# Optimization experiments

Hardware: AMD Instinct MI355X
Metric: run time of the kernel (lower is better)

## Reference

```python
import jax, jax.numpy as jnp
import numpy as np

DIM = 64
HEADS = 4
WIN = 4


def setup_inputs() -> dict:
    key = jax.random.key(0)
    ks = jax.random.split(key, 9)
    B, C, D, H, W = 2, DIM, 64, 64, 64
    x = jax.random.normal(ks[0], (B, C, D, H, W), dtype=jnp.float32)
    # 1x1x1 Conv3d == pointwise linear: weight [C_out, C_in], bias [C_out]
    def mk(kw, kb):
        return (jax.random.normal(kw, (C, C), dtype=jnp.float32) * 0.05,
                jax.random.normal(kb, (C,), dtype=jnp.float32) * 0.05)
    Wq, bq = mk(ks[1], ks[2])
    Wk, bk = mk(ks[3], ks[4])
    Wv, bv = mk(ks[5], ks[6])
    Wp, bp = mk(ks[7], ks[8])
    return {"x": x, "Wq": Wq, "bq": bq, "Wk": Wk, "bk": bk,
            "Wv": Wv, "bv": bv, "Wp": Wp, "bp": bp}


def reference(x, Wq, bq, Wk, bk, Wv, bv, Wp, bp):
    B, C, D, H, W = x.shape
    w = WIN
    heads = HEADS
    hd = C // heads
    L = w * w * w  # tokens per window (64)
    nd, nh, nw = D // w, H // w, W // w  # spatial dims are multiples of w -> no padding branch
    scale = hd ** -0.5

    # window partition: [B,C,D,H,W] -> [B*nd*nh*nw, C, L]
    xw = (x.reshape(B, C, nd, w, nh, w, nw, w)
            .transpose(0, 2, 4, 6, 1, 3, 5, 7)
            .reshape(B * nd * nh * nw, C, L))

    def pointwise(t, Wm, bm):  # 1x1x1 conv on flattened windows
        return jnp.einsum('ncl,oc->nol', t, Wm) + bm[None, :, None]

    q = pointwise(xw, Wq, bq).reshape(-1, heads, hd, L)
    k = pointwise(xw, Wk, bk).reshape(-1, heads, hd, L)
    v = pointwise(xw, Wv, bv).reshape(-1, heads, hd, L)

    # attn[n,h,i,j] = <q[:, :, :, i], k[:, :, :, j]> * scale ; softmax over j
    attn = jax.nn.softmax(jnp.einsum('nhdi,nhdj->nhij', q, k) * scale, axis=-1)
    # out = v @ attn^T  (dropout is identity in eval)
    out = jnp.einsum('nhdj,nhij->nhdi', v, attn)

    out = out.reshape(-1, C, L)
    out = pointwise(out, Wp, bp)

    # reverse window partition: [B*nd*nh*nw, C, L] -> [B,C,D,H,W]
    out = (out.reshape(B, nd, nh, nw, C, w, w, w)
              .transpose(0, 4, 1, 5, 2, 6, 3, 7)
              .reshape(B, C, D, H, W))
    return out
```

## Files before the change

kernel.cpp:

```cpp
#include <hip/hip_runtime.h>

typedef _Float16 f16;
typedef __attribute__((ext_vector_type(4))) _Float16 f16x4;
typedef __attribute__((ext_vector_type(8))) _Float16 f16x8;
typedef __attribute__((ext_vector_type(4))) float f32x4;

#define MFMA32(a,b,c) __builtin_amdgcn_mfma_f32_16x16x32_f16((a),(b),(c),0,0,0)
#define MFMA16(a,b,c) __builtin_amdgcn_mfma_f32_16x16x16f16((a),(b),(c),0,0,0)

__global__ void wprep(const float* __restrict__ Wq, const float* __restrict__ Wk,
                      const float* __restrict__ Wv, const float* __restrict__ Wp,
                      f16* __restrict__ ws)
{
    const int t = threadIdx.x;
    const int lane = t & 63;
    const float* Wm[4] = {Wq, Wk, Wv, Wp};
    #pragma unroll
    for (int j = 0; j < 8; ++j) {
        const int c = (t >> 6) * 8 + j;
        const int m = c >> 3, ob = (c >> 1) & 3, s = c & 1;
        const float* src = Wm[m] + (ob * 16 + (lane & 15)) * 64 + 8 * (lane >> 4) + 32 * s;
        f32x4 a4 = *(const f32x4*)src;
        f32x4 b4 = *(const f32x4*)(src + 4);
        f16x8 h;
        #pragma unroll
        for (int ii = 0; ii < 8; ++ii) h[ii] = (f16)(ii < 4 ? a4[ii] : b4[ii - 4]);
        *(f16x8*)(ws + c * 512 + lane * 8) = h;
    }
    #pragma unroll
    for (int j = 0; j < 4; ++j) {
        const int f = (t >> 6) * 4 + j;
        const int oc = f >> 2, hh = f & 3;
        f32x4 wv = *(const f32x4*)(Wp + (oc * 16 + (lane & 15)) * 64 + 16 * hh + 4 * (lane >> 4));
        f16x4 h4;
        #pragma unroll
        for (int r = 0; r < 4; ++r) h4[r] = (f16)wv[r];
        *(f16x4*)(ws + 16384 + f * 256 + lane * 4) = h4;
    }
}

__global__ __launch_bounds__(256, 3)
void wsa3d(const float* __restrict__ x, const f16* __restrict__ wsf,
           const float* __restrict__ bq, const float* __restrict__ bk,
           const float* __restrict__ bv, const float* __restrict__ bp,
           float* __restrict__ out)
{
    __shared__ __align__(16) f16 XW[16384];
    float* const SG = (float*)XW;

    const int tid  = threadIdx.x;
    const int lane = tid & 63;
    const int w    = tid >> 6;
    const int g    = lane >> 4;
    const int ln16 = lane & 15;
    const int key  = ln16 & 7;

    const int bid = blockIdx.x;
    const int Q   = ((bid & 7) << 8) | (bid >> 3);
    const int qx = Q & 3, ih = (Q >> 2) & 15, idz = (Q >> 6) & 15, b = Q >> 10;

    const float c_sc = 0.25f * 1.44269504088896340736f;
    const f32x4 z4 = {0.f, 0.f, 0.f, 0.f};
    const f16x4 ones = {(f16)1.f, (f16)1.f, (f16)1.f, (f16)1.f};

    const int gz = (lane >> 4) & 3, gy = (lane >> 2) & 3, gq = lane & 3;

    f16x4 valh[16];
    #pragma unroll
    for (int i = 0; i < 16; ++i) {
        const int c = w * 16 + i;
        f32x4 v4 = *(const f32x4*)(x + ((((b*64 + c)*64 + idz*4 + gz)*64) + ih*4 + gy)*64 + qx*16 + gq*4);
        #pragma unroll
        for (int r = 0; r < 4; ++r) valh[i][r] = (f16)v4[r];
    }

    #pragma unroll
    for (int lx = 0; lx < 4; ++lx) {
        const int t = gz * 16 + gy * 4 + lx;
        #pragma unroll
        for (int h2 = 0; h2 < 2; ++h2) {
            f16x8 pk;
            #pragma unroll
            for (int ii = 0; ii < 8; ++ii) pk[ii] = valh[h2 * 8 + ii][lx];
            *(f16x8*)(XW + gq*4096 + t*64 + (((w*2 + h2) ^ (t & 7) ^ gq) << 3)) = pk;
        }
    }
    __syncthreads();

    f16x8 xf[4][2];
    #pragma unroll
    for (int lb = 0; lb < 4; ++lb)
        #pragma unroll
        for (int s = 0; s < 2; ++s)
            xf[lb][s] = *(const f16x8*)(XW + w*4096 + (lb*16 + ln16)*64 + (((g + 4*s) ^ key ^ w) << 3));

    #pragma unroll
    for (int ob = 0; ob < 4; ++ob) {
        f16x8 VF[2];
        #pragma unroll
        for (int s = 0; s < 2; ++s) VF[s] = *(const f16x8*)(wsf + (16 + ob*2 + s)*512 + lane*8);
        const float bvo = bv[ob * 16 + ln16];
        #pragma unroll
        for (int tb = 0; tb < 4; ++tb) {
            f32x4 a = z4;
            #pragma unroll
            for (int s = 0; s < 2; ++s) a = MFMA32(xf[tb][s], VF[s], a);
            f16x4 h4;
            #pragma unroll
            for (int r = 0; r < 4; ++r) h4[r] = (f16)(a[r] + bvo);
            *(f16x4*)(XW + w*4096 + (ob*16 + ln16)*64 + (((2*tb + (g >> 1)) ^ key ^ w) << 3) + 4*(g & 1)) = h4;
        }
    }

    f16x4 ot[4][4];
    #pragma unroll
    for (int h = 0; h < 4; ++h) {
        f16x8 QF[2], KF[2];
        #pragma unroll
        for (int s = 0; s < 2; ++s) {
            QF[s] = *(const f16x8*)(wsf + (h*2 + s)*512 + lane*8);
            KF[s] = *(const f16x8*)(wsf + (8 + h*2 + s)*512 + lane*8);
        }
        const f32x4 bqv = *(const f32x4*)(bq + h*16 + g*4);
        const f32x4 bkv = *(const f32x4*)(bk + h*16 + g*4);
        f16x4 qf[4], kf[4];
        #pragma unroll
        for (int lb = 0; lb < 4; ++lb) {
            f32x4 aq = z4, ak = z4;
            #pragma unroll
            for (int s = 0; s < 2; ++s) {
                aq = MFMA32(QF[s], xf[lb][s], aq);
                ak = MFMA32(KF[s], xf[lb][s], ak);
            }
            #pragma unroll
            for (int r = 0; r < 4; ++r) {
                qf[lb][r] = (f16)((aq[r] + bqv[r]) * c_sc);
                kf[lb][r] = (f16)(ak[r] + bkv[r]);
            }
        }
        f16x4 va[4];
        #pragma unroll
        for (int jb = 0; jb < 4; ++jb)
            va[jb] = *(const f16x4*)(XW + w*4096 + (16*h + ln16)*64 + (((2*jb + (g >> 1)) ^ key ^ w) << 3) + 4*(g & 1));
        #pragma unroll
        for (int ib = 0; ib < 4; ++ib) {
            f16x4 pf[4];
            #pragma unroll
            for (int jb = 0; jb < 4; ++jb) {
                f32x4 S = MFMA16(kf[jb], qf[ib], z4);
                #pragma unroll
                for (int r = 0; r < 4; ++r) pf[jb][r] = (f16)__builtin_amdgcn_exp2f(S[r]);
            }
            f32x4 sm = z4;
            #pragma unroll
            for (int jb = 0; jb < 4; ++jb) sm = MFMA16(ones, pf[jb], sm);
            f32x4 O = z4;
            #pragma unroll
            for (int jb = 0; jb < 4; ++jb) O = MFMA16(va[jb], pf[jb], O);
            const float inv = __builtin_amdgcn_rcpf(sm[0]);
            #pragma unroll
            for (int r = 0; r < 4; ++r) ot[h][ib][r] = (f16)(O[r] * inv);
        }
    }
    __syncthreads();

    const f16* ws2 = wsf + 16384;
    #pragma unroll
    for (int half = 0; half < 2; ++half) {
        #pragma unroll
        for (int pp = 0; pp < 2; ++pp) {
            const int oc = half * 2 + pp;
            const float bpo = bp[oc * 16 + ln16];
            f16x4 wb[4];
            #pragma unroll
            for (int h = 0; h < 4; ++h)
                wb[h] = *(const f16x4*)(ws2 + (oc * 4 + h) * 256 + lane * 4);
            #pragma unroll
            for (int ib = 0; ib < 4; ++ib) {
                f32x4 a = z4;
                #pragma unroll
                for (int h = 0; h < 4; ++h) a = MFMA16(ot[h][ib], wb[h], a);
                #pragma unroll
                for (int r = 0; r < 4; ++r) a[r] += bpo;
                *(f32x4*)(SG + ((pp*4 + w)*16 + ln16)*64 + (((4*ib + g) ^ ln16 ^ w) << 2)) = a;
            }
        }
        __syncthreads();
        #pragma unroll
        for (int pp = 0; pp < 2; ++pp) {
            const int oc = half * 2 + pp;
            #pragma unroll
            for (int si = 0; si < 4; ++si) {
                const int o2 = w * 4 + si;
                f32x4 v4 = *(const f32x4*)(SG + ((pp*4 + gq)*16 + o2)*64 + (((gz*4 + gy) ^ o2 ^ gq) << 2));
                *(f32x4*)(out + ((((b*64 + oc*16 + o2)*64 + idz*4 + gz)*64) + ih*4 + gy)*64 + qx*16 + gq*4) = v4;
            }
        }
        if (half == 0) __syncthreads();
    }
}

extern "C" void kernel_launch(void* const* d_in, const int* in_sizes, int n_in,
                              void* d_out, int out_size, void* d_ws, size_t ws_size,
                              hipStream_t stream) {
    (void)in_sizes; (void)n_in; (void)out_size; (void)ws_size;
    const float* x  = (const float*)d_in[0];
    const float* Wq = (const float*)d_in[1];
    const float* bq = (const float*)d_in[2];
    const float* Wk = (const float*)d_in[3];
    const float* bk = (const float*)d_in[4];
    const float* Wv = (const float*)d_in[5];
    const float* bv = (const float*)d_in[6];
    const float* Wp = (const float*)d_in[7];
    const float* bp = (const float*)d_in[8];
    f16* wsf = (f16*)d_ws;
    wprep<<<1, 256, 0, stream>>>(Wq, Wk, Wv, Wp, wsf);
    wsa3d<<<2048, 256, 0, stream>>>(x, wsf, bq, bk, bv, bp, (float*)d_out);
}
```

Before: 72.86 us.

## Process two window groups per block and prefetch the second input during compute

Each block now handles two adjacent groups of windows (qx0 and qx1), halving the grid. The global loads for the second group are issued into registers while the first group's attention and projection are still running. The aim is to hide global load latency behind compute. In exchange, register pressure rises (32 extra f32x4 values live), which could lower occupancy or cause spills, and there are fewer blocks per GPU to hide latency.

```diff
diff --git a/kernel.cpp b/kernel.cpp
--- a/kernel.cpp
+++ b/kernel.cpp
@@ -38,6 +38,14 @@
         *(f16x4*)(ws + 16384 + f * 256 + lane * 4) = h4;
     }
 }
+
+#define GATHER16(RAW, B_, IDZ_, IH_, QX_)                                                     \
+    _Pragma("unroll")                                                                         \
+    for (int i = 0; i < 16; ++i) {                                                            \
+        const int c = w * 16 + i;                                                             \
+        RAW[i] = *(const f32x4*)(x + ((((B_*64 + c)*64 + IDZ_*4 + gz)*64) + IH_*4 + gy)*64    \
+                                   + QX_*16 + gq*4);                                          \
+    }
 
 __global__ __launch_bounds__(256, 3)
 void wsa3d(const float* __restrict__ x, const f16* __restrict__ wsf,
@@ -56,23 +64,23 @@
     const int key  = ln16 & 7;
 
     const int bid = blockIdx.x;
-    const int Q   = ((bid & 7) << 8) | (bid >> 3);
-    const int qx = Q & 3, ih = (Q >> 2) & 15, idz = (Q >> 6) & 15, b = Q >> 10;
+    const int Bp  = ((bid & 7) << 7) | (bid >> 3);
+    const int Q0  = Bp * 2;
+    const int qx0 = Q0 & 3, ih = (Q0 >> 2) & 15, idz = (Q0 >> 6) & 15, b = Q0 >> 10;
+    const int qx1 = qx0 | 1;
 
     const float c_sc = 0.25f * 1.44269504088896340736f;
     const f32x4 z4 = {0.f, 0.f, 0.f, 0.f};
     const f16x4 ones = {(f16)1.f, (f16)1.f, (f16)1.f, (f16)1.f};
+    const f16* ws2 = wsf + 16384;
 
     const int gz = (lane >> 4) & 3, gy = (lane >> 2) & 3, gq = lane & 3;
 
-    f16x4 valh[16];
-    #pragma unroll
-    for (int i = 0; i < 16; ++i) {
-        const int c = w * 16 + i;
-        f32x4 v4 = *(const f32x4*)(x + ((((b*64 + c)*64 + idz*4 + gz)*64) + ih*4 + gy)*64 + qx*16 + gq*4);
-        #pragma unroll
-        for (int r = 0; r < 4; ++r) valh[i][r] = (f16)v4[r];
-    }
+    f16x8 xf[4][2];
+    f16x4 ot[4][4];
+    f32x4 raw0[16], raw1[16];
+
+    GATHER16(raw0, b, idz, ih, qx0)
 
     #pragma unroll
     for (int lx = 0; lx < 4; ++lx) {
@@ -81,13 +89,12 @@
         for (int h2 = 0; h2 < 2; ++h2) {
             f16x8 pk;
             #pragma unroll
-            for (int ii = 0; ii < 8; ++ii) pk[ii] = valh[h2 * 8 + ii][lx];
+            for (int ii = 0; ii < 8; ++ii) pk[ii] = (f16)raw0[h2 * 8 + ii][lx];
             *(f16x8*)(XW + gq*4096 + t*64 + (((w*2 + h2) ^ (t & 7) ^ gq) << 3)) = pk;
         }
     }
     __syncthreads();
 
-    f16x8 xf[4][2];
     #pragma unroll
     for (int lb = 0; lb < 4; ++lb)
         #pragma unroll
@@ -112,7 +119,6 @@
         }
     }
 
-    f16x4 ot[4][4];
     #pragma unroll
     for (int h = 0; h < 4; ++h) {
         f16x8 QF[2], KF[2];
@@ -162,9 +168,11 @@
             for (int r = 0; r < 4; ++r) ot[h][ib][r] = (f16)(O[r] * inv);
         }
     }
+
+    GATHER16(raw1, b, idz, ih, qx1)
+
     __syncthreads();
 
-    const f16* ws2 = wsf + 16384;
     #pragma unroll
     for (int half = 0; half < 2; ++half) {
         #pragma unroll
@@ -193,7 +201,129 @@
             for (int si = 0; si < 4; ++si) {
                 const int o2 = w * 4 + si;
                 f32x4 v4 = *(const f32x4*)(SG + ((pp*4 + gq)*16 + o2)*64 + (((gz*4 + gy) ^ o2 ^ gq) << 2));
-                *(f32x4*)(out + ((((b*64 + oc*16 + o2)*64 + idz*4 + gz)*64) + ih*4 + gy)*64 + qx*16 + gq*4) = v4;
+                *(f32x4*)(out + ((((b*64 + oc*16 + o2)*64 + idz*4 + gz)*64) + ih*4 + gy)*64 + qx0*16 + gq*4) = v4;
+            }
+        }
+        __syncthreads();
+    }
+
+    #pragma unroll
+    for (int lx = 0; lx < 4; ++lx) {
+        const int t = gz * 16 + gy * 4 + lx;
+        #pragma unroll
+        for (int h2 = 0; h2 < 2; ++h2) {
+            f16x8 pk;
+            #pragma unroll
+            for (int ii = 0; ii < 8; ++ii) pk[ii] = (f16)raw1[h2 * 8 + ii][lx];
+            *(f16x8*)(XW + gq*4096 + t*64 + (((w*2 + h2) ^ (t & 7) ^ gq) << 3)) = pk;
+        }
+    }
+    __syncthreads();
+
+    #pragma unroll
+    for (int lb = 0; lb < 4; ++lb)
+        #pragma unroll
+        for (int s = 0; s < 2; ++s)
+            xf[lb][s] = *(const f16x8*)(XW + w*4096 + (lb*16 + ln16)*64 + (((g + 4*s) ^ key ^ w) << 3));
+
+    #pragma unroll
+    for (int ob = 0; ob < 4; ++ob) {
+        f16x8 VF[2];
+        #pragma unroll
+        for (int s = 0; s < 2; ++s) VF[s] = *(const f16x8*)(wsf + (16 + ob*2 + s)*512 + lane*8);
+        const float bvo = bv[ob * 16 + ln16];
+        #pragma unroll
+        for (int tb = 0; tb < 4; ++tb) {
+            f32x4 a = z4;
+            #pragma unroll
+            for (int s = 0; s < 2; ++s) a = MFMA32(xf[tb][s], VF[s], a);
+            f16x4 h4;
+            #pragma unroll
+            for (int r = 0; r < 4; ++r) h4[r] = (f16)(a[r] + bvo);
+            *(f16x4*)(XW + w*4096 + (ob*16 + ln16)*64 + (((2*tb + (g >> 1)) ^ key ^ w) << 3) + 4*(g & 1)) = h4;
+        }
+    }
+
+    #pragma unroll
+    for (int h = 0; h < 4; ++h) {
+        f16x8 QF[2], KF[2];
+        #pragma unroll
+        for (int s = 0; s < 2; ++s) {
+            QF[s] = *(const f16x8*)(wsf + (h*2 + s)*512 + lane*8);
+            KF[s] = *(const f16x8*)(wsf + (8 + h*2 + s)*512 + lane*8);
+        }
+        const f32x4 bqv = *(const f32x4*)(bq + h*16 + g*4);
+        const f32x4 bkv = *(const f32x4*)(bk + h*16 + g*4);
+        f16x4 qf[4], kf[4];
+        #pragma unroll
+        for (int lb = 0; lb < 4; ++lb) {
+            f32x4 aq = z4, ak = z4;
+            #pragma unroll
+            for (int s = 0; s < 2; ++s) {
+                aq = MFMA32(QF[s], xf[lb][s], aq);
+                ak = MFMA32(KF[s], xf[lb][s], ak);
+            }
+            #pragma unroll
+            for (int r = 0; r < 4; ++r) {
+                qf[lb][r] = (f16)((aq[r] + bqv[r]) * c_sc);
+                kf[lb][r] = (f16)(ak[r] + bkv[r]);
+            }
+        }
+        f16x4 va[4];
+        #pragma unroll
+        for (int jb = 0; jb < 4; ++jb)
+            va[jb] = *(const f16x4*)(XW + w*4096 + (16*h + ln16)*64 + (((2*jb + (g >> 1)) ^ key ^ w) << 3) + 4*(g & 1));
+        #pragma unroll
+        for (int ib = 0; ib < 4; ++ib) {
+            f16x4 pf[4];
+            #pragma unroll
+            for (int jb = 0; jb < 4; ++jb) {
+                f32x4 S = MFMA16(kf[jb], qf[ib], z4);
+                #pragma unroll
+                for (int r = 0; r < 4; ++r) pf[jb][r] = (f16)__builtin_amdgcn_exp2f(S[r]);
+            }
+            f32x4 sm = z4;
+            #pragma unroll
+            for (int jb = 0; jb < 4; ++jb) sm = MFMA16(ones, pf[jb], sm);
+            f32x4 O = z4;
+            #pragma unroll
+            for (int jb = 0; jb < 4; ++jb) O = MFMA16(va[jb], pf[jb], O);
+            const float inv = __builtin_amdgcn_rcpf(sm[0]);
+            #pragma unroll
+            for (int r = 0; r < 4; ++r) ot[h][ib][r] = (f16)(O[r] * inv);
+        }
+    }
+    __syncthreads();
+
+    #pragma unroll
+    for (int half = 0; half < 2; ++half) {
+        #pragma unroll
+        for (int pp = 0; pp < 2; ++pp) {
+            const int oc = half * 2 + pp;
+            const float bpo = bp[oc * 16 + ln16];
+            f16x4 wb[4];
+            #pragma unroll
+            for (int h = 0; h < 4; ++h)
+                wb[h] = *(const f16x4*)(ws2 + (oc * 4 + h) * 256 + lane * 4);
+            #pragma unroll
+            for (int ib = 0; ib < 4; ++ib) {
+                f32x4 a = z4;
+                #pragma unroll
+                for (int h = 0; h < 4; ++h) a = MFMA16(ot[h][ib], wb[h], a);
+                #pragma unroll
+                for (int r = 0; r < 4; ++r) a[r] += bpo;
+                *(f32x4*)(SG + ((pp*4 + w)*16 + ln16)*64 + (((4*ib + g) ^ ln16 ^ w) << 2)) = a;
+            }
+        }
+        __syncthreads();
+        #pragma unroll
+        for (int pp = 0; pp < 2; ++pp) {
+            const int oc = half * 2 + pp;
+            #pragma unroll
+            for (int si = 0; si < 4; ++si) {
+                const int o2 = w * 4 + si;
+                f32x4 v4 = *(const f32x4*)(SG + ((pp*4 + gq)*16 + o2)*64 + (((gz*4 + gy) ^ o2 ^ gq) << 2));
+                *(f32x4*)(out + ((((b*64 + oc*16 + o2)*64 + idz*4 + gz)*64) + ih*4 + gy)*64 + qx1*16 + gq*4) = v4;
             }
         }
         if (half == 0) __syncthreads();
@@ -215,5 +345,5 @@
     const float* bp = (const float*)d_in[8];
     f16* wsf = (f16*)d_ws;
     wprep<<<1, 256, 0, stream>>>(Wq, Wk, Wv, Wp, wsf);
-    wsa3d<<<2048, 256, 0, stream>>>(x, wsf, bq, bk, bv, bp, (float*)d_out);
+    wsa3d<<<1024, 256, 0, stream>>>(x, wsf, bq, bk, bv, bp, (float*)d_out);
 }
```

Result: slower. 113.7 us (+56.1%).
